# Performance work log

Hardware: AMD Instinct MI355X
Metric: run time of the kernel (lower is better)

Reference implementation:

```python
import jax, jax.numpy as jnp
import numpy as np
from jax import lax

DIM = 256
HEADS = 8
EPS = 1e-12  # torch F.normalize eps


def setup_inputs() -> dict:
    key = jax.random.key(0)
    ks = jax.random.split(key, 6)
    b, c, h, w = 2, DIM, 128, 128
    x = jax.random.normal(ks[0], (b, c, h, w), dtype=jnp.float32)
    # qkv 1x1 conv (no bias): weight [3*dim, dim]
    w_qkv = jax.random.normal(ks[1], (3 * c, c), dtype=jnp.float32) * (1.0 / np.sqrt(c))
    # depthwise 3x3 conv, groups = 3*dim: weight [3*dim, 1, 3, 3]
    w_dw = jax.random.normal(ks[2], (3 * c, 1, 3, 3), dtype=jnp.float32) * (1.0 / 3.0)
    # project_out 1x1 conv: [dim, dim]
    w_proj = jax.random.normal(ks[3], (c, c), dtype=jnp.float32) * (1.0 / np.sqrt(c))
    temperature = jnp.ones((HEADS, 1, 1), dtype=jnp.float32)
    a1 = jnp.full((1,), 0.2, dtype=jnp.float32)
    a2 = jnp.full((1,), 0.2, dtype=jnp.float32)
    a3 = jnp.full((1,), 0.2, dtype=jnp.float32)
    a4 = jnp.full((1,), 0.2, dtype=jnp.float32)
    return {"x": x, "w_qkv": w_qkv, "w_dw": w_dw, "w_proj": w_proj,
            "temperature": temperature, "a1": a1, "a2": a2, "a3": a3, "a4": a4}


def _l2norm(t):
    # torch F.normalize(dim=-1): t / max(||t||, eps)
    n = jnp.sqrt(jnp.sum(t * t, axis=-1, keepdims=True))
    return t / jnp.maximum(n, EPS)


def reference(x, w_qkv, w_dw, w_proj, temperature, a1, a2, a3, a4):
    b, c, h, w = x.shape
    heads = temperature.shape[0]
    C = c // heads
    hw = h * w
    # 1x1 conv then depthwise 3x3 conv (groups = 3c)
    qkv = jnp.einsum('oc,bchw->bohw', w_qkv, x)
    qkv = lax.conv_general_dilated(
        qkv, w_dw, window_strides=(1, 1), padding='SAME',
        dimension_numbers=('NCHW', 'OIHW', 'NCHW'), feature_group_count=3 * c)
    q, k, v = jnp.split(qkv, 3, axis=1)
    q = _l2norm(q.reshape(b, heads, C, hw))
    k = _l2norm(k.reshape(b, heads, C, hw))
    v = v.reshape(b, heads, C, hw)
    # channel attention: [b, heads, C, C]
    attn = jnp.einsum('bhcn,bhdn->bhcd', q, k) * temperature
    flat = attn.reshape(b, heads, C * C)
    # share one descending sort across all four top-k passes
    sorted_desc = jnp.sort(flat, axis=-1)[..., ::-1]
    N = C * C
    neg_inf = jnp.asarray(-jnp.inf, dtype=flat.dtype)

    def spar_softmax(topk):
        thresh = sorted_desc[..., topk - 1:topk]  # kth largest value
        masked = jnp.where(flat >= thresh, flat, neg_inf)
        return jax.nn.softmax(masked, axis=-1).reshape(b, heads, C, C)

    s1 = spar_softmax(N * 1 // 2)
    s2 = spar_softmax(N * 2 // 3)
    s3 = spar_softmax(N * 3 // 4)
    s4 = spar_softmax(N * 4 // 5)
    spar = s1 * a1 + s2 * a2 + s3 * a3 + s4 * a4
    out = jnp.einsum('bhcd,bhdn->bhcn', spar, v).reshape(b, c, h, w)
    out = jnp.einsum('oc,bchw->bohw', w_proj, out)
    return out
```

## Files before the change

### kernel.cpp

```cpp
#include <hip/hip_runtime.h>
#include <stdint.h>

#define HW     16384
#define IMGW   128
#define NCH    768
#define DIMC   256
#define NB     2
#define CPH    32

typedef unsigned short u16;
typedef unsigned int   u32;
typedef __attribute__((ext_vector_type(8))) short bf16x8;
typedef __attribute__((ext_vector_type(4))) float f32x4;

__device__ __forceinline__ float bf2f(u16 u) { return __uint_as_float(((u32)u) << 16); }
__device__ __forceinline__ u16 f2bf(float f) {
    u32 u = __float_as_uint(f);
    u += 0x7fffu + ((u >> 16) & 1u);
    return (u16)(u >> 16);
}

#define GLOAD16(gp, lp) __builtin_amdgcn_global_load_lds( \
    (const __attribute__((address_space(1))) void*)(gp),  \
    (__attribute__((address_space(3))) void*)(lp), 16, 0, 0)

__global__ __launch_bounds__(256)
void wsplit(const float* __restrict__ w, u16* __restrict__ wh, u16* __restrict__ wl)
{
    const int idx = blockIdx.x * 256 + threadIdx.x;
    const int m = idx >> 3, s = idx & 7;
    const int p = (m >> 1) & 3;
    #pragma unroll
    for (int u = 0; u < 4; ++u) {
        const int cb = s * 32 + ((u ^ p) << 3);
        u32 hq[4], lq[4];
        #pragma unroll
        for (int e2 = 0; e2 < 4; ++e2) {
            float f0 = w[m * 256 + cb + 2 * e2];
            float f1 = w[m * 256 + cb + 2 * e2 + 1];
            u16 h0 = f2bf(f0); u16 l0 = f2bf(f0 - bf2f(h0));
            u16 h1 = f2bf(f1); u16 l1 = f2bf(f1 - bf2f(h1));
            hq[e2] = (u32)h0 | ((u32)h1 << 16);
            lq[e2] = (u32)l0 | ((u32)l1 << 16);
        }
        size_t rowb = ((size_t)(s * 768 + m)) << 6;
        uint4 hv = {hq[0], hq[1], hq[2], hq[3]};
        uint4 lv = {lq[0], lq[1], lq[2], lq[3]};
        *(uint4*)((char*)wh + rowb + (u << 4)) = hv;
        *(uint4*)((char*)wl + rowb + (u << 4)) = lv;
    }
}

__global__ __launch_bounds__(256)
void transp_split(const float* __restrict__ src, long srcBatch,
                  u16* __restrict__ dsth, u16* __restrict__ dstl)
{
    __shared__ float Xs[64][68];
    const int bz = blockIdx.y;
    const int nt = blockIdx.x & 255;
    const int ct = blockIdx.x >> 8;
    const int n0 = nt * 64, c0 = ct * 64;
    const int t = threadIdx.x;
    const float* xb = src + (size_t)bz * srcBatch;

    #pragma unroll
    for (int it = 0; it < 4; ++it) {
        int cl = (t >> 4) + it * 16;
        int nl4 = (t & 15) << 2;
        float4 v = *(const float4*)(xb + (size_t)(c0 + cl) * HW + n0 + nl4);
        Xs[cl][nl4]     = v.x; Xs[cl][nl4 + 1] = v.y;
        Xs[cl][nl4 + 2] = v.z; Xs[cl][nl4 + 3] = v.w;
    }
    __syncthreads();

    const int nl = t >> 2, u = t & 3;
    const int p = (nl >> 1) & 3;
    #pragma unroll
    for (int sl = 0; sl < 2; ++sl) {
        const int s = (c0 >> 5) + sl;
        const int cb = sl * 32 + ((u ^ p) << 3);
        u32 hq[4], lq[4];
        #pragma unroll
        for (int e2 = 0; e2 < 4; ++e2) {
            float f0 = Xs[cb + 2 * e2][nl];
            float f1 = Xs[cb + 2 * e2 + 1][nl];
            u16 h0 = f2bf(f0); u16 l0 = f2bf(f0 - bf2f(h0));
            u16 h1 = f2bf(f1); u16 l1 = f2bf(f1 - bf2f(h1));
            hq[e2] = (u32)h0 | ((u32)h1 << 16);
            lq[e2] = (u32)l0 | ((u32)l1 << 16);
        }
        size_t rowb = ((size_t)((bz * 8 + s)) * 16384 + n0 + nl) << 6;
        uint4 hv = {hq[0], hq[1], hq[2], hq[3]};
        uint4 lv = {lq[0], lq[1], lq[2], lq[3]};
        *(uint4*)((char*)dsth + rowb + (u << 4)) = hv;
        *(uint4*)((char*)dstl + rowb + (u << 4)) = lv;
    }
}

template<bool FULLB, bool OUTBF16, int MBLKS>
__global__ __launch_bounds__(256, 2)
void gemm_mfma_split(const u16* __restrict__ Ahp, const u16* __restrict__ Alp,
                     const u16* __restrict__ Bhp, const u16* __restrict__ Blp,
                     void* __restrict__ Cp, int aBatch, int aSlice, long cBatch)
{
    constexpr int BUFSZ = FULLB ? 32768 : 24576;
    __shared__ char smem[2 * BUFSZ];

    const int t    = threadIdx.x;
    const int lane = t & 63;
    const int w    = t >> 6;
    const int per = gridDim.x >> 3;
    const int wid = (blockIdx.x & 7) * per + (blockIdx.x >> 3);
    const int nglob = wid / MBLKS;
    const int m0 = (wid % MBLKS) * 128;
    const int bz = nglob >> 7;
    const int n0 = (nglob & 127) * 128;

    const int lrow  = lane >> 2;
    const int lquad = lane & 3;
    const int mh = w >> 1, nh = w & 1;
    const int swz = ((lane & 15) << 6) + ((((lane >> 4) ^ ((lane >> 1) & 3))) << 4);

    f32x4 acc[4][4];
    #pragma unroll
    for (int i = 0; i < 4; ++i)
        #pragma unroll
        for (int j = 0; j < 4; ++j)
            acc[i][j] = (f32x4){0.f, 0.f, 0.f, 0.f};

    auto stage = [&](int buf, int s) {
        const size_t arow0 = (size_t)bz * aBatch + (size_t)s * aSlice + m0;
        const size_t brow0 = ((size_t)(bz * 8 + s)) * 16384 + n0;
        char* base = smem + buf * BUFSZ;
        constexpr int NCHK = FULLB ? 8 : 6;
        #pragma unroll
        for (int i = 0; i < NCHK; ++i) {
            const int tile = i >> 1;
            const int r16  = ((i & 1) << 2) | w;
            char* dst = base + tile * 8192 + r16 * 1024;
            const char* src;
            if (tile == 0)
                src = (const char*)Ahp + ((arow0 + r16 * 16 + lrow) << 6) + (lquad << 4);
            else if (tile == 1)
                src = (const char*)Alp + ((arow0 + r16 * 16 + lrow) << 6) + (lquad << 4);
            else if (tile == 2)
                src = (const char*)Bhp + ((brow0 + r16 * 16 + lrow) << 6) + (lquad << 4);
            else
                src = (const char*)Blp + ((brow0 + r16 * 16 + lrow) << 6) + (lquad << 4);
            GLOAD16(src, dst);
        }
    };

    stage(0, 0);
    __syncthreads();

    #pragma unroll
    for (int s = 0; s < 8; ++s) {
        char* base = smem + (s & 1) * BUFSZ;
        if (s < 7) stage((s + 1) & 1, s + 1);

        bf16x8 ah[4], al[4], bh[4], bl[4];
        #pragma unroll
        for (int f = 0; f < 4; ++f) {
            const int aoff = (mh * 64 + f * 16) * 64 + swz;
            ah[f] = *(const bf16x8*)(base + aoff);
            al[f] = *(const bf16x8*)(base + 8192 + aoff);
            const int boff = (nh * 64 + f * 16) * 64 + swz;
            bh[f] = *(const bf16x8*)(base + 16384 + boff);
            if (FULLB) bl[f] = *(const bf16x8*)(base + 24576 + boff);
        }

        #pragma unroll
        for (int fm = 0; fm < 4; ++fm)
            #pragma unroll
            for (int fn = 0; fn < 4; ++fn) {
                acc[fm][fn] = __builtin_amdgcn_mfma_f32_16x16x32_bf16(ah[fm], bh[fn], acc[fm][fn], 0, 0, 0);
                if (FULLB)
                    acc[fm][fn] = __builtin_amdgcn_mfma_f32_16x16x32_bf16(ah[fm], bl[fn], acc[fm][fn], 0, 0, 0);
                acc[fm][fn] = __builtin_amdgcn_mfma_f32_16x16x32_bf16(al[fm], bh[fn], acc[fm][fn], 0, 0, 0);
            }

        if (s < 7) __syncthreads();
    }

    #pragma unroll
    for (int fm = 0; fm < 4; ++fm) {
        const int mrow0 = m0 + mh * 64 + fm * 16 + ((lane >> 4) << 2);
        #pragma unroll
        for (int fn = 0; fn < 4; ++fn) {
            const int ncol = n0 + nh * 64 + fn * 16 + (lane & 15);
            if (OUTBF16) {
                u16* Cb = (u16*)Cp + (size_t)bz * cBatch;
                #pragma unroll
                for (int r = 0; r < 4; ++r)
                    Cb[(size_t)(mrow0 + r) * HW + ncol] = f2bf(acc[fm][fn][r]);
            } else {
                float* Cb = (float*)Cp + (size_t)bz * cBatch;
                #pragma unroll
                for (int r = 0; r < 4; ++r)
                    Cb[(size_t)(mrow0 + r) * HW + ncol] = acc[fm][fn][r];
            }
        }
    }
}

__global__ __launch_bounds__(256)
void dwconv3(const u16* __restrict__ in, const float* __restrict__ wdw,
             u16* __restrict__ out)
{
    const int y  = blockIdx.y;
    const int bi = y >> 9, ch = y & 511;
    const size_t p = (size_t)bi * NCH + ch;
    const int t  = threadIdx.x;
    const int r0 = blockIdx.x * 32 + (t >> 5) * 4;
    const int c0 = (t & 31) << 2;

    const u16* plane = in + p * HW;
    const float* wp = wdw + ch * 9;
    float w[9];
    #pragma unroll
    for (int i = 0; i < 9; ++i) w[i] = wp[i];

    float rv[6][6];
    #pragma unroll
    for (int j = 0; j < 6; ++j) {
        const int ry = r0 - 1 + j;
        if (ry < 0 || ry >= IMGW) {
            #pragma unroll
            for (int k = 0; k < 6; ++k) rv[j][k] = 0.f;
        } else {
            const u16* rp = plane + ry * IMGW;
            ushort4 vm = *(const ushort4*)(rp + c0);
            rv[j][0] = (c0 > 0)   ? bf2f(rp[c0 - 1]) : 0.f;
            rv[j][1] = bf2f(vm.x); rv[j][2] = bf2f(vm.y);
            rv[j][3] = bf2f(vm.z); rv[j][4] = bf2f(vm.w);
            rv[j][5] = (c0 < 124) ? bf2f(rp[c0 + 4]) : 0.f;
        }
    }

    #pragma unroll
    for (int rr = 0; rr < 4; ++rr) {
        float acc[4] = {0.f, 0.f, 0.f, 0.f};
        #pragma unroll
        for (int dy = 0; dy < 3; ++dy) {
            #pragma unroll
            for (int dx = 0; dx < 3; ++dx) {
                float wv = w[dy * 3 + dx];
                #pragma unroll
                for (int q = 0; q < 4; ++q)
                    acc[q] = fmaf(rv[rr + dy][q + dx], wv, acc[q]);
            }
        }
        ushort4 o4;
        o4.x = f2bf(acc[0]); o4.y = f2bf(acc[1]);
        o4.z = f2bf(acc[2]); o4.w = f2bf(acc[3]);
        *(ushort4*)(out + p * HW + (r0 + rr) * IMGW + c0) = o4;
    }
}

__global__ __launch_bounds__(256)
void dwconv_v(const u16* __restrict__ qkvb, const float* __restrict__ wdw,
              u16* __restrict__ vth)
{
    __shared__ u16 Lout[256][40];
    const int rp = blockIdx.x;
    const int s  = blockIdx.y;
    const int bz = blockIdx.z;
    const int t  = threadIdx.x;
    const int ch = t >> 3;
    const int cg = t & 7;
    const int r0 = rp * 2;
    const int c0 = cg * 16;
    const int chg = 512 + s * 32 + ch;
    const u16* plane = qkvb + ((size_t)bz * NCH + chg) * HW;
    const float* wp = wdw + chg * 9;
    float w[9];
    #pragma unroll
    for (int i = 0; i < 9; ++i) w[i] = wp[i];

    float rv[4][18];
    #pragma unroll
    for (int j = 0; j < 4; ++j) {
        const int ry = r0 - 1 + j;
        if (ry < 0 || ry >= IMGW) {
            #pragma unroll
            for (int k = 0; k < 18; ++k) rv[j][k] = 0.f;
        } else {
            const u16* rw = plane + ry * IMGW;
            bf16x8 v0 = *(const bf16x8*)(rw + c0);
            bf16x8 v1 = *(const bf16x8*)(rw + c0 + 8);
            rv[j][0] = (c0 > 0) ? bf2f(rw[c0 - 1]) : 0.f;
            #pragma unroll
            for (int e = 0; e < 8; ++e) {
                rv[j][1 + e] = bf2f((u16)v0[e]);
                rv[j][9 + e] = bf2f((u16)v1[e]);
            }
            rv[j][17] = (c0 < 112) ? bf2f(rw[c0 + 16]) : 0.f;
        }
    }

    #pragma unroll
    for (int rr = 0; rr < 2; ++rr) {
        float acc[16];
        #pragma unroll
        for (int q = 0; q < 16; ++q) acc[q] = 0.f;
        #pragma unroll
        for (int dy = 0; dy < 3; ++dy)
            #pragma unroll
            for (int dx = 0; dx < 3; ++dx) {
                float wv = w[dy * 3 + dx];
                #pragma unroll
                for (int q = 0; q < 16; ++q)
                    acc[q] = fmaf(rv[rr + dy][q + dx], wv, acc[q]);
            }
        #pragma unroll
        for (int q = 0; q < 16; ++q)
            Lout[rr * 128 + c0 + q][ch] = f2bf(acc[q]);
    }
    __syncthreads();

    u16* dst = vth + (((size_t)(bz * 8 + s)) * 16384 + rp * 256 + t) * 32;
    const int pq = (t >> 1) & 3;
    #pragma unroll
    for (int u = 0; u < 4; ++u)
        *(uint4*)(dst + u * 8) = *(const uint4*)(&Lout[t][(u ^ pq) * 8]);
}

__global__ __launch_bounds__(256)
void gram_mfma(const u16* __restrict__ dw, float* __restrict__ part,
               float* __restrict__ sumsqp)
{
    __shared__ float pl[4][32][32];
    __shared__ float sl[4][64];
    const int chunk = blockIdx.x;
    const int bh    = blockIdx.y;
    const int bi = bh >> 3, h = bh & 7;
    const u16* qbase = dw + ((size_t)bi * NCH + h * CPH) * HW;
    const u16* kbase = dw + ((size_t)bi * NCH + 256 + h * CPH) * HW;
    const int t = threadIdx.x, lane = t & 63, w = t >> 6;
    const int lr = lane & 15;
    const int lg = lane >> 4;

    f32x4 acc[2][2];
    #pragma unroll
    for (int i = 0; i < 2; ++i)
        #pragma unroll
        for (int j = 0; j < 2; ++j)
            acc[i][j] = (f32x4){0.f, 0.f, 0.f, 0.f};
    float sq[4] = {0.f, 0.f, 0.f, 0.f};

    #pragma unroll
    for (int ks = 0; ks < 4; ++ks) {
        const int nb = chunk * 512 + w * 128 + ks * 32 + lg * 8;
        bf16x8 a0 = *(const bf16x8*)(qbase + (size_t)lr * HW + nb);
        bf16x8 a1 = *(const bf16x8*)(qbase + (size_t)(lr + 16) * HW + nb);
        bf16x8 b0 = *(const bf16x8*)(kbase + (size_t)lr * HW + nb);
        bf16x8 b1 = *(const bf16x8*)(kbase + (size_t)(lr + 16) * HW + nb);
        acc[0][0] = __builtin_amdgcn_mfma_f32_16x16x32_bf16(a0, b0, acc[0][0], 0, 0, 0);
        acc[0][1] = __builtin_amdgcn_mfma_f32_16x16x32_bf16(a0, b1, acc[0][1], 0, 0, 0);
        acc[1][0] = __builtin_amdgcn_mfma_f32_16x16x32_bf16(a1, b0, acc[1][0], 0, 0, 0);
        acc[1][1] = __builtin_amdgcn_mfma_f32_16x16x32_bf16(a1, b1, acc[1][1], 0, 0, 0);
        #pragma unroll
        for (int e = 0; e < 8; ++e) {
            float f0 = bf2f((u16)a0[e]); sq[0] = fmaf(f0, f0, sq[0]);
            float f1 = bf2f((u16)a1[e]); sq[1] = fmaf(f1, f1, sq[1]);
            float f2 = bf2f((u16)b0[e]); sq[2] = fmaf(f2, f2, sq[2]);
            float f3 = bf2f((u16)b1[e]); sq[3] = fmaf(f3, f3, sq[3]);
        }
    }
    #pragma unroll
    for (int i = 0; i < 4; ++i) {
        sq[i] += __shfl_xor(sq[i], 16);
        sq[i] += __shfl_xor(sq[i], 32);
    }
    if (lane < 16) {
        sl[w][lane]      = sq[0];
        sl[w][16 + lane] = sq[1];
        sl[w][32 + lane] = sq[2];
        sl[w][48 + lane] = sq[3];
    }
    #pragma unroll
    for (int qt = 0; qt < 2; ++qt)
        #pragma unroll
        for (int kt = 0; kt < 2; ++kt)
            #pragma unroll
            for (int r = 0; r < 4; ++r)
                pl[w][qt * 16 + lg * 4 + r][kt * 16 + lr] = acc[qt][kt][r];
    __syncthreads();

    #pragma unroll
    for (int i = 0; i < 4; ++i) {
        const int o = i * 256 + t;
        const int qc = o >> 5, kd = o & 31;
        float s = pl[0][qc][kd] + pl[1][qc][kd] + pl[2][qc][kd] + pl[3][qc][kd];
        part[((size_t)chunk * 16 + bh) * 1024 + o] = s;
    }
    if (t < 64) {
        float s = sl[0][t] + sl[1][t] + sl[2][t] + sl[3][t];
        sumsqp[((size_t)chunk * 16 + bh) * 64 + t] = s;
    }
}

__global__ __launch_bounds__(1024)
void softfin(const float* __restrict__ part, const float* __restrict__ sumsqp,
             const float* __restrict__ temp, float* __restrict__ spar,
             const float* __restrict__ a1, const float* __restrict__ a2,
             const float* __restrict__ a3, const float* __restrict__ a4)
{
    __shared__ float xs[1024];
    __shared__ float red[16 * 4];
    __shared__ float vthr[4];
    __shared__ float msh;
    __shared__ float ssh[4];

    const int bh = blockIdx.x, t = threadIdx.x;
    const int h = bh & 7;
    const int c = t >> 5, d = t & 31;
    const int idx = bh * 1024 + t;

    float s = 0.f, sqq = 0.f, sqk = 0.f;
    #pragma unroll
    for (int ch = 0; ch < 32; ++ch) {
        s   += part[(size_t)ch * 16384 + idx];
        sqq += sumsqp[((size_t)ch * 16 + bh) * 64 + c];
        sqk += sumsqp[((size_t)ch * 16 + bh) * 64 + 32 + d];
    }
    float iq = 1.f / fmaxf(sqrtf(sqq), 1e-12f);
    float ik = 1.f / fmaxf(sqrtf(sqk), 1e-12f);
    float x = s * iq * ik * temp[h];
    xs[t] = x;
    __syncthreads();

    int g = 0, e = 0;
    const float4* xs4 = (const float4*)xs;
    for (int j = 0; j < 256; ++j) {
        float4 v = xs4[j];
        g += (v.x > x) + (v.y > x) + (v.z > x) + (v.w > x);
        e += (v.x == x) + (v.y == x) + (v.z == x) + (v.w == x);
    }
    if (g == 0) msh = x;
    const int topks[4] = {512, 682, 768, 819};
    #pragma unroll
    for (int kk = 0; kk < 4; ++kk)
        if (g <= topks[kk] - 1 && topks[kk] - 1 < g + e) vthr[kk] = x;
    __syncthreads();

    float m  = msh;
    float ex = expf(x - m);
    float v4[4];
    #pragma unroll
    for (int kk = 0; kk < 4; ++kk) v4[kk] = (x >= vthr[kk]) ? ex : 0.f;
    #pragma unroll
    for (int off = 32; off; off >>= 1)
        #pragma unroll
        for (int kk = 0; kk < 4; ++kk) v4[kk] += __shfl_down(v4[kk], off);
    const int lane = t & 63, wid = t >> 6;
    if (lane == 0) {
        #pragma unroll
        for (int kk = 0; kk < 4; ++kk) red[wid * 4 + kk] = v4[kk];
    }
    __syncthreads();
    if (t == 0) {
        float s0 = 0, s1 = 0, s2 = 0, s3 = 0;
        for (int ww = 0; ww < 16; ++ww) {
            s0 += red[ww * 4 + 0]; s1 += red[ww * 4 + 1];
            s2 += red[ww * 4 + 2]; s3 += red[ww * 4 + 3];
        }
        ssh[0] = s0; ssh[1] = s1; ssh[2] = s2; ssh[3] = s3;
    }
    __syncthreads();

    float av[4] = {*a1, *a2, *a3, *a4};
    float coef = 0.f;
    #pragma unroll
    for (int kk = 0; kk < 4; ++kk)
        if (x >= vthr[kk]) coef += av[kk] / ssh[kk];
    spar[bh * 1024 + t] = ex * coef;
}

__global__ __launch_bounds__(256)
void build_m2_split(const float* __restrict__ wproj, const float* __restrict__ spar,
                    u16* __restrict__ m2h, u16* __restrict__ m2l)
{
    const int idx = blockIdx.x * 256 + threadIdx.x;
    const int b = idx >> 16, o = (idx >> 8) & 255, hd = idx & 255;
    const int h = hd >> 5, d = hd & 31;
    const float* wrow = wproj + o * 256 + h * CPH;
    const float* sp = spar + (size_t)(b * 8 + h) * 1024 + d;
    float acc = 0.f;
    #pragma unroll 8
    for (int cc = 0; cc < 32; ++cc)
        acc = fmaf(wrow[cc], sp[cc * 32], acc);
    u16 hi = f2bf(acc);
    u16 lo = f2bf(acc - bf2f(hi));
    const int s = hd >> 5, cslot = hd & 31;
    const int qt = cslot >> 3, e = cslot & 7;
    const int p = (o >> 1) & 3;
    size_t pos = ((size_t)(b * 2048 + s * 256 + o) << 5) + ((qt ^ p) << 3) + e;
    m2h[pos] = hi;
    m2l[pos] = lo;
}

extern "C" void kernel_launch(void* const* d_in, const int* in_sizes, int n_in,
                              void* d_out, int out_size, void* d_ws, size_t ws_size,
                              hipStream_t stream)
{
    const float* x      = (const float*)d_in[0];
    const float* w_qkv  = (const float*)d_in[1];
    const float* w_dw   = (const float*)d_in[2];
    const float* w_proj = (const float*)d_in[3];
    const float* temp   = (const float*)d_in[4];
    const float* a1     = (const float*)d_in[5];
    const float* a2     = (const float*)d_in[6];
    const float* a3     = (const float*)d_in[7];
    const float* a4     = (const float*)d_in[8];

    float* ws = (float*)d_ws;
    u16* qkvb = (u16*)ws;
    u16* vth  = (u16*)(ws + 12582912);
    float* sumsqp = ws;
    float* part = ws + 32768;
    float* spar = ws + 32768 + 524288;
    u16* m2h = (u16*)(spar + 16384);
    u16* m2l = m2h + 131072;
    float* r1 = ws + (size_t)25165824;
    u16* xth = (u16*)r1;
    u16* xtl = xth + (size_t)8388608;
    u16* whp = xtl + (size_t)8388608;
    u16* wlp = whp + (size_t)196608;
    u16* dwb = (u16*)r1;

    wsplit<<<24, 256, 0, stream>>>(w_qkv, whp, wlp);
    transp_split<<<dim3(1024, 2), 256, 0, stream>>>(x, (long)DIMC * HW, xth, xtl);
    gemm_mfma_split<true, true, 6><<<1536, 256, 0, stream>>>(
        whp, wlp, xth, xtl, qkvb, 0, 768, (long)NCH * HW);
    dwconv3<<<dim3(4, NB * 512), 256, 0, stream>>>(qkvb, w_dw, dwb);
    dwconv_v<<<dim3(64, 8, NB), 256, 0, stream>>>(qkvb, w_dw, vth);
    gram_mfma<<<dim3(32, 16), 256, 0, stream>>>(dwb, part, sumsqp);
    softfin<<<16, 1024, 0, stream>>>(part, sumsqp, temp, spar, a1, a2, a3, a4);
    build_m2_split<<<512, 256, 0, stream>>>(w_proj, spar, m2h, m2l);
    gemm_mfma_split<false, false, 2><<<512, 256, 0, stream>>>(
        m2h, m2l, vth, nullptr, d_out, 2048, 256, (long)DIMC * HW);
}
```

Measured before the change: 149.1 us.

## Split softmax finish into gram-finish, parallel rank, and apply kernels

The single 16-block softfin kernel is split into three kernels. A 64-block kernel finalizes normalized attention, a 128-block kernel computes ranks and thresholds in parallel, and a 16-block kernel applies the masked softmaxes. This spreads the O(N^2) rank counting over many more CUs than the old 16 blocks used. In exchange it adds two kernel launches and a small global round trip for the attention matrix and thresholds.

```diff
diff --git a/kernel.cpp b/kernel.cpp
--- a/kernel.cpp
+++ b/kernel.cpp
@@ -401,23 +401,14 @@
     }
 }
 
-__global__ __launch_bounds__(1024)
-void softfin(const float* __restrict__ part, const float* __restrict__ sumsqp,
-             const float* __restrict__ temp, float* __restrict__ spar,
-             const float* __restrict__ a1, const float* __restrict__ a2,
-             const float* __restrict__ a3, const float* __restrict__ a4)
-{
-    __shared__ float xs[1024];
-    __shared__ float red[16 * 4];
-    __shared__ float vthr[4];
-    __shared__ float msh;
-    __shared__ float ssh[4];
-
-    const int bh = blockIdx.x, t = threadIdx.x;
+__global__ __launch_bounds__(256)
+void gram_finish(const float* __restrict__ part, const float* __restrict__ sumsqp,
+                 const float* __restrict__ temp, float* __restrict__ attn)
+{
+    const int idx = blockIdx.x * 256 + threadIdx.x;
+    const int bh = idx >> 10;
     const int h = bh & 7;
-    const int c = t >> 5, d = t & 31;
-    const int idx = bh * 1024 + t;
-
+    const int c = (idx >> 5) & 31, d = idx & 31;
     float s = 0.f, sqq = 0.f, sqk = 0.f;
     #pragma unroll
     for (int ch = 0; ch < 32; ++ch) {
@@ -427,10 +418,22 @@
     }
     float iq = 1.f / fmaxf(sqrtf(sqq), 1e-12f);
     float ik = 1.f / fmaxf(sqrtf(sqk), 1e-12f);
-    float x = s * iq * ik * temp[h];
-    xs[t] = x;
-    __syncthreads();
-
+    attn[idx] = s * iq * ik * temp[h];
+}
+
+__global__ __launch_bounds__(128)
+void rank4(const float* __restrict__ attn, float* __restrict__ vthr_g)
+{
+    __shared__ float xs[1024];
+    const int seg = blockIdx.x, bh = blockIdx.y;
+    const int t = threadIdx.x;
+    const float* row = attn + bh * 1024;
+
+    *(float4*)(&xs[t * 8])     = *(const float4*)(row + t * 8);
+    *(float4*)(&xs[t * 8 + 4]) = *(const float4*)(row + t * 8 + 4);
+    __syncthreads();
+
+    const float x = xs[seg * 128 + t];
     int g = 0, e = 0;
     const float4* xs4 = (const float4*)xs;
     for (int j = 0; j < 256; ++j) {
@@ -438,14 +441,28 @@
         g += (v.x > x) + (v.y > x) + (v.z > x) + (v.w > x);
         e += (v.x == x) + (v.y == x) + (v.z == x) + (v.w == x);
     }
-    if (g == 0) msh = x;
+    if (g == 0) vthr_g[bh * 8 + 4] = x;
     const int topks[4] = {512, 682, 768, 819};
     #pragma unroll
     for (int kk = 0; kk < 4; ++kk)
-        if (g <= topks[kk] - 1 && topks[kk] - 1 < g + e) vthr[kk] = x;
-    __syncthreads();
-
-    float m  = msh;
+        if (g <= topks[kk] - 1 && topks[kk] - 1 < g + e) vthr_g[bh * 8 + kk] = x;
+}
+
+__global__ __launch_bounds__(1024)
+void apply_soft(const float* __restrict__ attn, const float* __restrict__ vthr_g,
+                float* __restrict__ spar,
+                const float* __restrict__ a1, const float* __restrict__ a2,
+                const float* __restrict__ a3, const float* __restrict__ a4)
+{
+    __shared__ float red[16 * 4];
+    __shared__ float ssh[4];
+    const int bh = blockIdx.x, t = threadIdx.x;
+    const float x = attn[bh * 1024 + t];
+    float vthr[4];
+    #pragma unroll
+    for (int kk = 0; kk < 4; ++kk) vthr[kk] = vthr_g[bh * 8 + kk];
+    const float m = vthr_g[bh * 8 + 4];
+
     float ex = expf(x - m);
     float v4[4];
     #pragma unroll
@@ -519,9 +536,11 @@
     u16* qkvb = (u16*)ws;
     u16* vth  = (u16*)(ws + 12582912);
     float* sumsqp = ws;
-    float* part = ws + 32768;
-    float* spar = ws + 32768 + 524288;
-    u16* m2h = (u16*)(spar + 16384);
+    float* part   = ws + 32768;
+    float* attn   = ws + 557056;
+    float* spar   = ws + 573440;
+    float* vthr_g = ws + 589824;
+    u16* m2h = (u16*)(ws + 589952);
     u16* m2l = m2h + 131072;
     float* r1 = ws + (size_t)25165824;
     u16* xth = (u16*)r1;
@@ -537,7 +556,9 @@
     dwconv3<<<dim3(4, NB * 512), 256, 0, stream>>>(qkvb, w_dw, dwb);
     dwconv_v<<<dim3(64, 8, NB), 256, 0, stream>>>(qkvb, w_dw, vth);
     gram_mfma<<<dim3(32, 16), 256, 0, stream>>>(dwb, part, sumsqp);
-    softfin<<<16, 1024, 0, stream>>>(part, sumsqp, temp, spar, a1, a2, a3, a4);
+    gram_finish<<<64, 256, 0, stream>>>(part, sumsqp, temp, attn);
+    rank4<<<dim3(8, 16), 128, 0, stream>>>(attn, vthr_g);
+    apply_soft<<<16, 1024, 0, stream>>>(attn, vthr_g, spar, a1, a2, a3, a4);
     build_m2_split<<<512, 256, 0, stream>>>(w_proj, spar, m2h, m2l);
     gemm_mfma_split<false, false, 2><<<512, 256, 0, stream>>>(
         m2h, m2l, vth, nullptr, d_out, 2048, 256, (long)DIMC * HW);
```

Measured after the change: 133.8 us. 10.3% less time.
